# Kernel optimization log

Hardware: AMD Instinct MI355X
Metric: run time of the kernel (lower is better)

The kernel has to match this reference:

```python
import jax, jax.numpy as jnp
import numpy as np

B, D, H = 512, 32, 256
N_STEPS = 8
T0, T1 = 0.0, 1.0

# Dopri5 Butcher tableau (5th-order solution weights; k7 weight is 0 so 6 stages suffice)
_C = (0.0, 1.0 / 5, 3.0 / 10, 4.0 / 5, 8.0 / 9, 1.0)
_A = (
    (),
    (1.0 / 5,),
    (3.0 / 40, 9.0 / 40),
    (44.0 / 45, -56.0 / 15, 32.0 / 9),
    (19372.0 / 6561, -25360.0 / 2187, 64448.0 / 6561, -212.0 / 729),
    (9017.0 / 3168, -355.0 / 33, 46732.0 / 5247, 49.0 / 176, -5103.0 / 18656),
)
_B = (35.0 / 384, 0.0, 500.0 / 1113, 125.0 / 192, -2187.0 / 6784, 11.0 / 84)


def setup_inputs() -> dict:
    key = jax.random.key(0)
    ks = jax.random.split(key, 7)
    s1 = 1.0 / np.sqrt(D + 1)
    s2 = 1.0 / np.sqrt(H)
    return {
        "x": jax.random.normal(ks[0], (B, D), jnp.float32),
        "W1": (jax.random.normal(ks[1], (D + 1, H)) * s1).astype(jnp.float32),
        "b1": jnp.zeros((H,), jnp.float32),
        "W2": (jax.random.normal(ks[2], (H, H)) * s2).astype(jnp.float32),
        "b2": jnp.zeros((H,), jnp.float32),
        "W3": (jax.random.normal(ks[3], (H, D)) * s2).astype(jnp.float32),
        "b3": jnp.zeros((D,), jnp.float32),
    }


def _vf(t, x, W1, b1, W2, b2, W3, b3):
    # time-conditioned MLP vector field: input_shape == output_shape == (D,)
    h = jnp.concatenate([x, jnp.reshape(t, (1,)).astype(x.dtype)])
    h = jnp.tanh(h @ W1 + b1)
    h = jnp.tanh(h @ W2 + b2)
    return h @ W3 + b3


def _vf_and_trace(t, x, params):
    # exact Jacobian via D vmapped JVPs against identity, as in the original module
    apply_vf = lambda xx: _vf(t, xx, *params)
    eye = jnp.eye(D, dtype=x.dtype)
    dxdt_all, J = jax.vmap(lambda v: jax.jvp(apply_vf, (x,), (v,)))(eye)
    dxdt = dxdt_all[0]
    return dxdt, jnp.trace(J), jnp.sum(J * J)


def _deriv(t, carry, params):
    # forward (inverse=False) direction: t -> t1 - t, dxdt negated
    x, log_det, vf_norm, jac_frob = carry
    t_eff = T1 - t
    dxdt, tr, frob = jax.vmap(lambda xx: _vf_and_trace(t_eff, xx, params))(x)
    dxdt = -dxdt
    return (dxdt, -tr, jnp.sum(dxdt * dxdt, axis=-1), frob)


def _solve(x, params):
    dt = (T1 - T0) / N_STEPS
    zeros = jnp.zeros((x.shape[0],), x.dtype)
    y0 = (x, zeros, zeros, zeros)

    def step(carry, t):
        ks = []
        for i in range(6):
            if i == 0:
                yi = carry
            else:
                a = _A[i]
                yi = jax.tree_util.tree_map(
                    lambda y, *kk: y + dt * sum(c * k for c, k in zip(a, kk)),
                    carry, *ks)
            ks.append(_deriv(t + _C[i] * dt, yi, params))
        y_new = jax.tree_util.tree_map(
            lambda y, *kk: y + dt * sum(c * k for c, k in zip(_B, kk)),
            carry, *ks)
        return y_new, None

    ts = T0 + dt * jnp.arange(N_STEPS, dtype=x.dtype)
    (z, log_det, vf_norm, jac_frob), _ = jax.lax.scan(step, y0, ts)
    # pack (z, log_det, total_vf_norm, total_jac_frob_norm) into one array: (B, D+3)
    return jnp.concatenate(
        [z, log_det[:, None], vf_norm[:, None], jac_frob[:, None]], axis=-1)


def reference(x, W1, b1, W2, b2, W3, b3):
    return _solve(x, (W1, b1, W2, b2, W3, b3))
```

## Files before the change

kernel.cpp:

```cpp
#include <hip/hip_runtime.h>

#define NB 512
#define ND 32
#define NH 256
#define NSTEPS 8

typedef __attribute__((ext_vector_type(8))) short short8;
typedef __attribute__((ext_vector_type(4))) short short4v;
typedef __attribute__((ext_vector_type(4))) float f32x4;

__device__ __constant__ float Atab[6][5] = {
    {0.f, 0.f, 0.f, 0.f, 0.f},
    {0.2f, 0.f, 0.f, 0.f, 0.f},
    {3.f/40.f, 9.f/40.f, 0.f, 0.f, 0.f},
    {44.f/45.f, -56.f/15.f, 32.f/9.f, 0.f, 0.f},
    {19372.f/6561.f, -25360.f/2187.f, 64448.f/6561.f, -212.f/729.f, 0.f},
    {9017.f/3168.f, -355.f/33.f, 46732.f/5247.f, 49.f/176.f, -5103.f/18656.f}
};
__device__ __constant__ float Btab[6] = {
    35.f/384.f, 0.f, 500.f/1113.f, 125.f/192.f, -2187.f/6784.f, 11.f/84.f
};
__device__ __constant__ float Ctab[6] = {0.f, 0.2f, 0.3f, 0.8f, 8.f/9.f, 1.f};

static __device__ __forceinline__ short f2bf(float f){
    __bf16 h = (__bf16)f;
    return __builtin_bit_cast(short, h);
}
static __device__ __forceinline__ float bf_lo(unsigned p){
    return __builtin_bit_cast(float, p << 16);
}
static __device__ __forceinline__ float bf_hi(unsigned p){
    return __builtin_bit_cast(float, p & 0xffff0000u);
}
static __device__ __forceinline__ float fast_tanh(float x){
    float e = __expf(2.f * x);
    return 1.f - 2.f / (e + 1.f);
}

#define SWZ(base, row, byte) ((base) + ((row) << 9) + ((byte) ^ (((row) & 7) << 4)))

extern "C" __global__ void prep_kernel(const float* __restrict__ W3,
                                       short8* __restrict__ ws)
{
    const int tid = threadIdx.x;
    #pragma unroll
    for (int r = 0; r < 4; ++r) {
        const int idx = r*256 + tid;
        const int l  = idx & 63;
        const int kk = (idx >> 6) & 7;
        const int mt = idx >> 9;
        const int g = (l >> 4) & 3, c = l & 15;
        short8 v;
        #pragma unroll
        for (int e = 0; e < 8; ++e)
            v[e] = f2bf(W3[(kk*32 + g*8 + e)*ND + mt*16 + c]);
        ws[idx] = v;
    }
}

extern "C" __global__ void __launch_bounds__(256, 2)
node_kernel(const float* __restrict__ x_in,
            const float* __restrict__ W1, const float* __restrict__ b1,
            const float* __restrict__ W2, const float* __restrict__ b2,
            const float* __restrict__ W3, const float* __restrict__ b3,
            const short8* __restrict__ w3ws,
            float* __restrict__ out)
{
    __shared__ __align__(16) short LAA[33*256];
    __shared__ __align__(16) short LTs[33*256];
    __shared__ __align__(16) short8 W3L[16*64];
    __shared__ __align__(16) unsigned LW1[16*256];
    __shared__ __align__(16) float h2pre_s[NH];
    __shared__ __align__(16) float s2_s[NH];
    __shared__ __align__(16) float xs_s[4][ND];
    __shared__ __align__(16) float xc_s[4][ND];
    __shared__ __align__(16) float ksb[4][6][ND];
    __shared__ float red[4][3];

    const int bid = blockIdx.x;
    const int tid = threadIdx.x;
    const int w = tid >> 6;
    const int l = tid & 63;
    const int g = (tid >> 4) & 3;
    const int c = tid & 15;

    char* LAc = (char*)LAA;
    char* LTc = (char*)LTs;
    const int swc = (c & 7) << 4;

    short8 w2f[4][8];
    #pragma unroll
    for (int m = 0; m < 4; ++m) {
        const int j = w*64 + m*16 + c;
        #pragma unroll
        for (int kk = 0; kk < 8; ++kk) {
            const int k0 = kk*32 + g*8;
            short8 f;
            #pragma unroll
            for (int e = 0; e < 8; ++e) f[e] = f2bf(W2[(k0+e)*NH + j]);
            w2f[m][kk] = f;
        }
    }
    float w1t, b1u, b2u;
    {
        #pragma unroll
        for (int q = 0; q < 16; ++q) {
            unsigned lo = (unsigned)(unsigned short)f2bf(W1[(2*q)*NH + tid]);
            unsigned hi = (unsigned)(unsigned short)f2bf(W1[(2*q+1)*NH + tid]);
            LW1[q*256 + tid] = lo | (hi << 16);
        }
        w1t = W1[32*NH + tid];
        b1u = b1[tid];
        b2u = b2[tid];
    }
    const f32x4 b3a = *(const f32x4*)(b3 + g*4);
    const f32x4 b3b = *(const f32x4*)(b3 + 16 + g*4);
    #pragma unroll
    for (int r = 0; r < 4; ++r) W3L[r*256 + tid] = w3ws[r*256 + tid];
    const int mtJ = w >> 1, ntJ = w & 1;

    if (l < ND) {
        const float xv = x_in[bid*ND + l];
        xc_s[w][l] = xv;
        xs_s[w][l] = xv;
    }
    __syncthreads();

    const float dt = 0.125f;
    float fr_acc = 0.f, ld_acc = 0.f, vf_acc = 0.f;
    const short8 zfrag = {0,0,0,0,0,0,0,0};

    for (int n = 0; n < NSTEPS; ++n) {
        const float t0 = (float)n * dt;
        for (int sg = 0; sg < 6; ++sg) {
            const float t_eff = 1.0f - (t0 + Ctab[sg]*dt);

            {
                float pre = b1u + t_eff * w1t;
                #pragma unroll
                for (int q = 0; q < 8; ++q) {
                    f32x4 xq = *(const f32x4*)&xs_s[w][q*4];
                    unsigned p0 = LW1[(2*q)*256 + tid];
                    unsigned p1 = LW1[(2*q+1)*256 + tid];
                    pre += xq[0]*bf_lo(p0) + xq[1]*bf_hi(p0)
                         + xq[2]*bf_lo(p1) + xq[3]*bf_hi(p1);
                }
                const float h1 = fast_tanh(pre);
                const float s1 = 1.f - h1*h1;
                #pragma unroll
                for (int q = 0; q < 16; ++q) {
                    unsigned p = LW1[q*256 + tid];
                    *(short*)SWZ(LAc, 2*q,   2*tid) = f2bf(bf_lo(p)*s1);
                    *(short*)SWZ(LAc, 2*q+1, 2*tid) = f2bf(bf_hi(p)*s1);
                }
                ((short*)LAA)[32*256 + tid] = f2bf(h1);
            }
            __syncthreads();

            {
                f32x4 acc2[4];
                #pragma unroll
                for (int m = 0; m < 4; ++m) acc2[m] = (f32x4){0.f,0.f,0.f,0.f};
                #pragma unroll
                for (int kk = 0; kk < 8; ++kk) {
                    const int bo = kk*64 + g*16;
                    short8 fA2 = zfrag;
                    if (c == 0) fA2 = *(const short8*)(LAc + (32 << 9) + bo);
                    #pragma unroll
                    for (int m = 0; m < 4; ++m)
                        acc2[m] = __builtin_amdgcn_mfma_f32_16x16x32_bf16(w2f[m][kk], fA2, acc2[m], 0,0,0);
                }
                if (c == 0) {
                    #pragma unroll
                    for (int m = 0; m < 4; ++m)
                        *(f32x4*)&h2pre_s[w*64 + m*16 + g*4] = acc2[m];
                }
            }
            const float h2 = fast_tanh(h2pre_s[tid] + b2u);
            s2_s[tid] = 1.f - h2*h2;
            ((short*)LTs)[32*256 + tid] = f2bf(h2);

            #pragma unroll 1
            for (int nt = 0; nt < 2; ++nt) {
                f32x4 accT[4];
                #pragma unroll
                for (int m = 0; m < 4; ++m) accT[m] = (f32x4){0.f,0.f,0.f,0.f};
                #pragma unroll
                for (int kk = 0; kk < 8; ++kk) {
                    const int bo = kk*64 + g*16;
                    short8 fA = *(const short8*)(LAc + ((nt*16 + c) << 9) + (bo ^ swc));
                    #pragma unroll
                    for (int m = 0; m < 4; ++m)
                        accT[m] = __builtin_amdgcn_mfma_f32_16x16x32_bf16(w2f[m][kk], fA, accT[m], 0,0,0);
                }
                #pragma unroll
                for (int m = 0; m < 4; ++m) {
                    const int j0 = w*64 + m*16 + g*4;
                    f32x4 s2q = *(const f32x4*)&s2_s[j0];
                    f32x4 v = accT[m] * s2q;
                    short4v p;
                    p[0] = f2bf(v[0]); p[1] = f2bf(v[1]); p[2] = f2bf(v[2]); p[3] = f2bf(v[3]);
                    *(short4v*)SWZ(LTc, nt*16 + c, 2*j0) = p;
                }
            }
            __syncthreads();

            f32x4 jva = (f32x4){0,0,0,0}, jvb = (f32x4){0,0,0,0}, jj = (f32x4){0,0,0,0};
            #pragma unroll
            for (int kk = 0; kk < 8; ++kk) {
                const int bo = kk*64 + g*16;
                short8 w3f0 = W3L[kk*64 + l];
                short8 w3f1 = W3L[(8+kk)*64 + l];
                short8 h2f = zfrag;
                if (c == 0) h2f = *(const short8*)(LTc + (32 << 9) + bo);
                jva = __builtin_amdgcn_mfma_f32_16x16x32_bf16(w3f0, h2f, jva, 0,0,0);
                jvb = __builtin_amdgcn_mfma_f32_16x16x32_bf16(w3f1, h2f, jvb, 0,0,0);
                short8 bJ = *(const short8*)(LTc + ((ntJ*16 + c) << 9) + (bo ^ swc));
                jj = __builtin_amdgcn_mfma_f32_16x16x32_bf16((mtJ == 0) ? w3f0 : w3f1, bJ, jj, 0,0,0);
            }

            const float wB = dt * Btab[sg];
            if (c == 0) {
                f32x4 dxa, dxb;
                dxa[0] = -(jva[0]+b3a[0]); dxa[1] = -(jva[1]+b3a[1]);
                dxa[2] = -(jva[2]+b3a[2]); dxa[3] = -(jva[3]+b3a[3]);
                dxb[0] = -(jvb[0]+b3b[0]); dxb[1] = -(jvb[1]+b3b[1]);
                dxb[2] = -(jvb[2]+b3b[2]); dxb[3] = -(jvb[3]+b3b[3]);
                *(f32x4*)&ksb[w][sg][g*4]      = dxa;
                *(f32x4*)&ksb[w][sg][16 + g*4] = dxb;
                if (w == 3)
                    vf_acc += wB * (dxa[0]*dxa[0]+dxa[1]*dxa[1]+dxa[2]*dxa[2]+dxa[3]*dxa[3]
                                  + dxb[0]*dxb[0]+dxb[1]*dxb[1]+dxb[2]*dxb[2]+dxb[3]*dxb[3]);
            }
            if (l < ND) {
                if (sg < 5) {
                    float v = xc_s[w][l];
                    for (int q = 0; q <= sg; ++q) v += dt * Atab[sg+1][q] * ksb[w][q][l];
                    xs_s[w][l] = v;
                } else {
                    float v = xc_s[w][l];
                    #pragma unroll
                    for (int q = 0; q < 6; ++q) v += dt * Btab[q] * ksb[w][q][l];
                    xc_s[w][l] = v;
                    xs_s[w][l] = v;
                }
            }
            fr_acc += wB * (jj[0]*jj[0]+jj[1]*jj[1]+jj[2]*jj[2]+jj[3]*jj[3]);
            if (mtJ == ntJ) {
                const int dd = c - g*4;
                if (dd >= 0 && dd < 4) {
                    float da = (dd==0)?jj[0]:(dd==1)?jj[1]:(dd==2)?jj[2]:jj[3];
                    ld_acc -= wB * da;
                }
            }
        }
    }

    float fr = fr_acc, ld = ld_acc, vf = vf_acc;
    #pragma unroll
    for (int off = 32; off > 0; off >>= 1) {
        fr += __shfl_down(fr, off, 64);
        ld += __shfl_down(ld, off, 64);
        vf += __shfl_down(vf, off, 64);
    }
    if (l == 0) { red[w][0] = fr; red[w][1] = ld; red[w][2] = vf; }
    __syncthreads();
    if (tid == 0) {
        float a = 0.f, b = 0.f, cq = 0.f;
        #pragma unroll
        for (int q = 0; q < 4; ++q) { a += red[q][0]; b += red[q][1]; cq += red[q][2]; }
        out[bid*35 + 32] = b;
        out[bid*35 + 33] = cq;
        out[bid*35 + 34] = a;
    }
    if (w == 3 && l < ND) out[bid*35 + l] = xc_s[3][l];
}

extern "C" void kernel_launch(void* const* d_in, const int* in_sizes, int n_in,
                              void* d_out, int out_size, void* d_ws, size_t ws_size,
                              hipStream_t stream) {
    const float* x  = (const float*)d_in[0];
    const float* W1 = (const float*)d_in[1];
    const float* b1 = (const float*)d_in[2];
    const float* W2 = (const float*)d_in[3];
    const float* b2 = (const float*)d_in[4];
    const float* W3 = (const float*)d_in[5];
    const float* b3 = (const float*)d_in[6];
    float* outp = (float*)d_out;
    hipLaunchKernelGGL(prep_kernel, dim3(1), dim3(256), 0, stream,
                       W3, (short8*)d_ws);
    hipLaunchKernelGGL(node_kernel, dim3(NB), dim3(256), 0, stream,
                       x, W1, b1, W2, b2, W3, b3, (const short8*)d_ws, outp);
}
```

Measured before the change: 219.0 us.

## Process two samples per block with software-pipelined interleaved RK stages

Each block now handles two batch samples instead of one and interleaves their RK stage phases (alpha, beta1, beta2), so one sample's elementwise work overlaps the other's MFMA work between barriers. Shared buffers are doubled per sample, W3 fragments move from LDS into registers, and the grid is halved with launch bounds set to one block per SM. This aims to cut barrier stalls and serial dependency latency per stage. In exchange it raises register and LDS pressure and halves the grid to 256 blocks, which may leave CUs underused.

```diff
diff --git a/kernel.cpp b/kernel.cpp
--- a/kernel.cpp
+++ b/kernel.cpp
@@ -58,7 +58,7 @@
     }
 }
 
-extern "C" __global__ void __launch_bounds__(256, 2)
+extern "C" __global__ void __launch_bounds__(256, 1)
 node_kernel(const float* __restrict__ x_in,
             const float* __restrict__ W1, const float* __restrict__ b1,
             const float* __restrict__ W2, const float* __restrict__ b2,
@@ -66,16 +66,15 @@
             const short8* __restrict__ w3ws,
             float* __restrict__ out)
 {
-    __shared__ __align__(16) short LAA[33*256];
-    __shared__ __align__(16) short LTs[33*256];
-    __shared__ __align__(16) short8 W3L[16*64];
+    __shared__ __align__(16) short LAA[2][33*256];
+    __shared__ __align__(16) short LTs[2][33*256];
     __shared__ __align__(16) unsigned LW1[16*256];
-    __shared__ __align__(16) float h2pre_s[NH];
-    __shared__ __align__(16) float s2_s[NH];
-    __shared__ __align__(16) float xs_s[4][ND];
-    __shared__ __align__(16) float xc_s[4][ND];
-    __shared__ __align__(16) float ksb[4][6][ND];
-    __shared__ float red[4][3];
+    __shared__ __align__(16) float h2p[2][NH];
+    __shared__ __align__(16) float s2s[2][NH];
+    __shared__ __align__(16) float xss[4][2][ND];
+    __shared__ __align__(16) float xcs[4][2][ND];
+    __shared__ __align__(16) float ksb[4][2][6][ND];
+    __shared__ float red[4][6];
 
     const int bid = blockIdx.x;
     const int tid = threadIdx.x;
@@ -84,8 +83,6 @@
     const int g = (tid >> 4) & 3;
     const int c = tid & 15;
 
-    char* LAc = (char*)LAA;
-    char* LTc = (char*)LTs;
     const int swc = (c & 7) << 4;
 
     short8 w2f[4][8];
@@ -115,165 +112,202 @@
     }
     const f32x4 b3a = *(const f32x4*)(b3 + g*4);
     const f32x4 b3b = *(const f32x4*)(b3 + 16 + g*4);
+    short8 w3f0[8], w3f1[8];
     #pragma unroll
-    for (int r = 0; r < 4; ++r) W3L[r*256 + tid] = w3ws[r*256 + tid];
+    for (int kk = 0; kk < 8; ++kk) {
+        w3f0[kk] = w3ws[kk*64 + l];
+        w3f1[kk] = w3ws[(8+kk)*64 + l];
+    }
     const int mtJ = w >> 1, ntJ = w & 1;
 
     if (l < ND) {
-        const float xv = x_in[bid*ND + l];
-        xc_s[w][l] = xv;
-        xs_s[w][l] = xv;
+        const float x0 = x_in[(2*bid+0)*ND + l];
+        const float x1 = x_in[(2*bid+1)*ND + l];
+        xcs[w][0][l] = x0; xss[w][0][l] = x0;
+        xcs[w][1][l] = x1; xss[w][1][l] = x1;
     }
     __syncthreads();
 
     const float dt = 0.125f;
-    float fr_acc = 0.f, ld_acc = 0.f, vf_acc = 0.f;
+    float fr_a[2] = {0.f, 0.f}, ld_a[2] = {0.f, 0.f}, vf_a[2] = {0.f, 0.f};
     const short8 zfrag = {0,0,0,0,0,0,0,0};
 
-    for (int n = 0; n < NSTEPS; ++n) {
-        const float t0 = (float)n * dt;
-        for (int sg = 0; sg < 6; ++sg) {
-            const float t_eff = 1.0f - (t0 + Ctab[sg]*dt);
-
-            {
-                float pre = b1u + t_eff * w1t;
-                #pragma unroll
-                for (int q = 0; q < 8; ++q) {
-                    f32x4 xq = *(const f32x4*)&xs_s[w][q*4];
-                    unsigned p0 = LW1[(2*q)*256 + tid];
-                    unsigned p1 = LW1[(2*q+1)*256 + tid];
-                    pre += xq[0]*bf_lo(p0) + xq[1]*bf_hi(p0)
-                         + xq[2]*bf_lo(p1) + xq[3]*bf_hi(p1);
-                }
-                const float h1 = fast_tanh(pre);
-                const float s1 = 1.f - h1*h1;
-                #pragma unroll
-                for (int q = 0; q < 16; ++q) {
-                    unsigned p = LW1[q*256 + tid];
-                    *(short*)SWZ(LAc, 2*q,   2*tid) = f2bf(bf_lo(p)*s1);
-                    *(short*)SWZ(LAc, 2*q+1, 2*tid) = f2bf(bf_hi(p)*s1);
-                }
-                ((short*)LAA)[32*256 + tid] = f2bf(h1);
-            }
-            __syncthreads();
-
-            {
-                f32x4 acc2[4];
-                #pragma unroll
-                for (int m = 0; m < 4; ++m) acc2[m] = (f32x4){0.f,0.f,0.f,0.f};
-                #pragma unroll
-                for (int kk = 0; kk < 8; ++kk) {
-                    const int bo = kk*64 + g*16;
-                    short8 fA2 = zfrag;
-                    if (c == 0) fA2 = *(const short8*)(LAc + (32 << 9) + bo);
-                    #pragma unroll
-                    for (int m = 0; m < 4; ++m)
-                        acc2[m] = __builtin_amdgcn_mfma_f32_16x16x32_bf16(w2f[m][kk], fA2, acc2[m], 0,0,0);
-                }
-                if (c == 0) {
-                    #pragma unroll
-                    for (int m = 0; m < 4; ++m)
-                        *(f32x4*)&h2pre_s[w*64 + m*16 + g*4] = acc2[m];
-                }
-            }
-            const float h2 = fast_tanh(h2pre_s[tid] + b2u);
-            s2_s[tid] = 1.f - h2*h2;
-            ((short*)LTs)[32*256 + tid] = f2bf(h2);
-
-            #pragma unroll 1
-            for (int nt = 0; nt < 2; ++nt) {
-                f32x4 accT[4];
-                #pragma unroll
-                for (int m = 0; m < 4; ++m) accT[m] = (f32x4){0.f,0.f,0.f,0.f};
-                #pragma unroll
-                for (int kk = 0; kk < 8; ++kk) {
-                    const int bo = kk*64 + g*16;
-                    short8 fA = *(const short8*)(LAc + ((nt*16 + c) << 9) + (bo ^ swc));
-                    #pragma unroll
-                    for (int m = 0; m < 4; ++m)
-                        accT[m] = __builtin_amdgcn_mfma_f32_16x16x32_bf16(w2f[m][kk], fA, accT[m], 0,0,0);
-                }
-                #pragma unroll
-                for (int m = 0; m < 4; ++m) {
-                    const int j0 = w*64 + m*16 + g*4;
-                    f32x4 s2q = *(const f32x4*)&s2_s[j0];
-                    f32x4 v = accT[m] * s2q;
-                    short4v p;
-                    p[0] = f2bf(v[0]); p[1] = f2bf(v[1]); p[2] = f2bf(v[2]); p[3] = f2bf(v[3]);
-                    *(short4v*)SWZ(LTc, nt*16 + c, 2*j0) = p;
-                }
-            }
-            __syncthreads();
-
-            f32x4 jva = (f32x4){0,0,0,0}, jvb = (f32x4){0,0,0,0}, jj = (f32x4){0,0,0,0};
+    auto alpha = [&](int e, float t_eff) {
+        char* LAc = (char*)LAA[e];
+        float pre = b1u + t_eff * w1t;
+        #pragma unroll
+        for (int q = 0; q < 8; ++q) {
+            f32x4 xq = *(const f32x4*)&xss[w][e][q*4];
+            unsigned p0 = LW1[(2*q)*256 + tid];
+            unsigned p1 = LW1[(2*q+1)*256 + tid];
+            pre += xq[0]*bf_lo(p0) + xq[1]*bf_hi(p0)
+                 + xq[2]*bf_lo(p1) + xq[3]*bf_hi(p1);
+        }
+        const float h1 = fast_tanh(pre);
+        const float s1 = 1.f - h1*h1;
+        #pragma unroll
+        for (int q = 0; q < 16; ++q) {
+            unsigned p = LW1[q*256 + tid];
+            *(short*)SWZ(LAc, 2*q,   2*tid) = f2bf(bf_lo(p)*s1);
+            *(short*)SWZ(LAc, 2*q+1, 2*tid) = f2bf(bf_hi(p)*s1);
+        }
+        ((short*)LAA[e])[32*256 + tid] = f2bf(h1);
+    };
+
+    auto beta1 = [&](int e) {
+        char* LAc = (char*)LAA[e];
+        char* LTc = (char*)LTs[e];
+        {
+            f32x4 acc2[4];
+            #pragma unroll
+            for (int m = 0; m < 4; ++m) acc2[m] = (f32x4){0.f,0.f,0.f,0.f};
             #pragma unroll
             for (int kk = 0; kk < 8; ++kk) {
                 const int bo = kk*64 + g*16;
-                short8 w3f0 = W3L[kk*64 + l];
-                short8 w3f1 = W3L[(8+kk)*64 + l];
-                short8 h2f = zfrag;
-                if (c == 0) h2f = *(const short8*)(LTc + (32 << 9) + bo);
-                jva = __builtin_amdgcn_mfma_f32_16x16x32_bf16(w3f0, h2f, jva, 0,0,0);
-                jvb = __builtin_amdgcn_mfma_f32_16x16x32_bf16(w3f1, h2f, jvb, 0,0,0);
-                short8 bJ = *(const short8*)(LTc + ((ntJ*16 + c) << 9) + (bo ^ swc));
-                jj = __builtin_amdgcn_mfma_f32_16x16x32_bf16((mtJ == 0) ? w3f0 : w3f1, bJ, jj, 0,0,0);
-            }
-
-            const float wB = dt * Btab[sg];
+                short8 fA2 = zfrag;
+                if (c == 0) fA2 = *(const short8*)(LAc + (32 << 9) + bo);
+                #pragma unroll
+                for (int m = 0; m < 4; ++m)
+                    acc2[m] = __builtin_amdgcn_mfma_f32_16x16x32_bf16(w2f[m][kk], fA2, acc2[m], 0,0,0);
+            }
             if (c == 0) {
-                f32x4 dxa, dxb;
-                dxa[0] = -(jva[0]+b3a[0]); dxa[1] = -(jva[1]+b3a[1]);
-                dxa[2] = -(jva[2]+b3a[2]); dxa[3] = -(jva[3]+b3a[3]);
-                dxb[0] = -(jvb[0]+b3b[0]); dxb[1] = -(jvb[1]+b3b[1]);
-                dxb[2] = -(jvb[2]+b3b[2]); dxb[3] = -(jvb[3]+b3b[3]);
-                *(f32x4*)&ksb[w][sg][g*4]      = dxa;
-                *(f32x4*)&ksb[w][sg][16 + g*4] = dxb;
-                if (w == 3)
-                    vf_acc += wB * (dxa[0]*dxa[0]+dxa[1]*dxa[1]+dxa[2]*dxa[2]+dxa[3]*dxa[3]
-                                  + dxb[0]*dxb[0]+dxb[1]*dxb[1]+dxb[2]*dxb[2]+dxb[3]*dxb[3]);
-            }
-            if (l < ND) {
-                if (sg < 5) {
-                    float v = xc_s[w][l];
-                    for (int q = 0; q <= sg; ++q) v += dt * Atab[sg+1][q] * ksb[w][q][l];
-                    xs_s[w][l] = v;
-                } else {
-                    float v = xc_s[w][l];
-                    #pragma unroll
-                    for (int q = 0; q < 6; ++q) v += dt * Btab[q] * ksb[w][q][l];
-                    xc_s[w][l] = v;
-                    xs_s[w][l] = v;
-                }
-            }
-            fr_acc += wB * (jj[0]*jj[0]+jj[1]*jj[1]+jj[2]*jj[2]+jj[3]*jj[3]);
-            if (mtJ == ntJ) {
-                const int dd = c - g*4;
-                if (dd >= 0 && dd < 4) {
-                    float da = (dd==0)?jj[0]:(dd==1)?jj[1]:(dd==2)?jj[2]:jj[3];
-                    ld_acc -= wB * da;
-                }
-            }
-        }
-    }
-
-    float fr = fr_acc, ld = ld_acc, vf = vf_acc;
+                #pragma unroll
+                for (int m = 0; m < 4; ++m)
+                    *(f32x4*)&h2p[e][w*64 + m*16 + g*4] = acc2[m];
+            }
+        }
+        const float h2 = fast_tanh(h2p[e][tid] + b2u);
+        s2s[e][tid] = 1.f - h2*h2;
+        ((short*)LTs[e])[32*256 + tid] = f2bf(h2);
+        #pragma unroll 1
+        for (int nt = 0; nt < 2; ++nt) {
+            f32x4 accT[4];
+            #pragma unroll
+            for (int m = 0; m < 4; ++m) accT[m] = (f32x4){0.f,0.f,0.f,0.f};
+            #pragma unroll
+            for (int kk = 0; kk < 8; ++kk) {
+                const int bo = kk*64 + g*16;
+                short8 fA = *(const short8*)(LAc + ((nt*16 + c) << 9) + (bo ^ swc));
+                #pragma unroll
+                for (int m = 0; m < 4; ++m)
+                    accT[m] = __builtin_amdgcn_mfma_f32_16x16x32_bf16(w2f[m][kk], fA, accT[m], 0,0,0);
+            }
+            #pragma unroll
+            for (int m = 0; m < 4; ++m) {
+                const int j0 = w*64 + m*16 + g*4;
+                f32x4 s2q = *(const f32x4*)&s2s[e][j0];
+                f32x4 v = accT[m] * s2q;
+                short4v p;
+                p[0] = f2bf(v[0]); p[1] = f2bf(v[1]); p[2] = f2bf(v[2]); p[3] = f2bf(v[3]);
+                *(short4v*)SWZ(LTc, nt*16 + c, 2*j0) = p;
+            }
+        }
+    };
+
+    auto beta2 = [&](int e, int sg, float wB) {
+        char* LTc = (char*)LTs[e];
+        f32x4 jva = (f32x4){0,0,0,0}, jvb = (f32x4){0,0,0,0}, jj = (f32x4){0,0,0,0};
+        #pragma unroll
+        for (int kk = 0; kk < 8; ++kk) {
+            const int bo = kk*64 + g*16;
+            short8 h2f = zfrag;
+            if (c == 0) h2f = *(const short8*)(LTc + (32 << 9) + bo);
+            jva = __builtin_amdgcn_mfma_f32_16x16x32_bf16(w3f0[kk], h2f, jva, 0,0,0);
+            jvb = __builtin_amdgcn_mfma_f32_16x16x32_bf16(w3f1[kk], h2f, jvb, 0,0,0);
+            short8 bJ = *(const short8*)(LTc + ((ntJ*16 + c) << 9) + (bo ^ swc));
+            jj = __builtin_amdgcn_mfma_f32_16x16x32_bf16((mtJ == 0) ? w3f0[kk] : w3f1[kk], bJ, jj, 0,0,0);
+        }
+        if (c == 0) {
+            f32x4 dxa, dxb;
+            dxa[0] = -(jva[0]+b3a[0]); dxa[1] = -(jva[1]+b3a[1]);
+            dxa[2] = -(jva[2]+b3a[2]); dxa[3] = -(jva[3]+b3a[3]);
+            dxb[0] = -(jvb[0]+b3b[0]); dxb[1] = -(jvb[1]+b3b[1]);
+            dxb[2] = -(jvb[2]+b3b[2]); dxb[3] = -(jvb[3]+b3b[3]);
+            *(f32x4*)&ksb[w][e][sg][g*4]      = dxa;
+            *(f32x4*)&ksb[w][e][sg][16 + g*4] = dxb;
+            if (w == 3)
+                vf_a[e] += wB * (dxa[0]*dxa[0]+dxa[1]*dxa[1]+dxa[2]*dxa[2]+dxa[3]*dxa[3]
+                               + dxb[0]*dxb[0]+dxb[1]*dxb[1]+dxb[2]*dxb[2]+dxb[3]*dxb[3]);
+        }
+        if (l < ND) {
+            if (sg < 5) {
+                float v = xcs[w][e][l];
+                for (int q = 0; q <= sg; ++q) v += dt * Atab[sg+1][q] * ksb[w][e][q][l];
+                xss[w][e][l] = v;
+            } else {
+                float v = xcs[w][e][l];
+                #pragma unroll
+                for (int q = 0; q < 6; ++q) v += dt * Btab[q] * ksb[w][e][q][l];
+                xcs[w][e][l] = v;
+                xss[w][e][l] = v;
+            }
+        }
+        fr_a[e] += wB * (jj[0]*jj[0]+jj[1]*jj[1]+jj[2]*jj[2]+jj[3]*jj[3]);
+        if (mtJ == ntJ) {
+            const int dd = c - g*4;
+            if (dd >= 0 && dd < 4) {
+                float da = (dd==0)?jj[0]:(dd==1)?jj[1]:(dd==2)?jj[2]:jj[3];
+                ld_a[e] -= wB * da;
+            }
+        }
+    };
+
+    auto teff_of = [&](int s) {
+        const int n = s / 6, sg = s % 6;
+        return 1.0f - ((float)n * dt + Ctab[sg] * dt);
+    };
+
+    alpha(0, teff_of(0));
+    __syncthreads();
+    #pragma unroll 1
+    for (int s = 0; s < NSTEPS*6; ++s) {
+        const int sg = s % 6;
+        const float wB = dt * Btab[sg];
+        if (s > 0) beta2(1, (s-1) % 6, dt * Btab[(s-1) % 6]);
+        alpha(1, teff_of(s));
+        beta1(0);
+        __syncthreads();
+        beta2(0, sg, wB);
+        if (s < NSTEPS*6 - 1) alpha(0, teff_of(s+1));
+        beta1(1);
+        __syncthreads();
+    }
+    beta2(1, 5, dt * Btab[5]);
+
+    float r0 = fr_a[0], r1 = ld_a[0], r2 = vf_a[0];
+    float r3 = fr_a[1], r4 = ld_a[1], r5 = vf_a[1];
     #pragma unroll
     for (int off = 32; off > 0; off >>= 1) {
-        fr += __shfl_down(fr, off, 64);
-        ld += __shfl_down(ld, off, 64);
-        vf += __shfl_down(vf, off, 64);
-    }
-    if (l == 0) { red[w][0] = fr; red[w][1] = ld; red[w][2] = vf; }
+        r0 += __shfl_down(r0, off, 64);
+        r1 += __shfl_down(r1, off, 64);
+        r2 += __shfl_down(r2, off, 64);
+        r3 += __shfl_down(r3, off, 64);
+        r4 += __shfl_down(r4, off, 64);
+        r5 += __shfl_down(r5, off, 64);
+    }
+    if (l == 0) {
+        red[w][0]=r0; red[w][1]=r1; red[w][2]=r2;
+        red[w][3]=r3; red[w][4]=r4; red[w][5]=r5;
+    }
     __syncthreads();
     if (tid == 0) {
-        float a = 0.f, b = 0.f, cq = 0.f;
-        #pragma unroll
-        for (int q = 0; q < 4; ++q) { a += red[q][0]; b += red[q][1]; cq += red[q][2]; }
-        out[bid*35 + 32] = b;
-        out[bid*35 + 33] = cq;
-        out[bid*35 + 34] = a;
-    }
-    if (w == 3 && l < ND) out[bid*35 + l] = xc_s[3][l];
+        float a0=0,b0=0,c0=0,a1=0,b1v=0,c1=0;
+        #pragma unroll
+        for (int q = 0; q < 4; ++q) {
+            a0+=red[q][0]; b0+=red[q][1]; c0+=red[q][2];
+            a1+=red[q][3]; b1v+=red[q][4]; c1+=red[q][5];
+        }
+        out[(2*bid+0)*35 + 32] = b0;
+        out[(2*bid+0)*35 + 33] = c0;
+        out[(2*bid+0)*35 + 34] = a0;
+        out[(2*bid+1)*35 + 32] = b1v;
+        out[(2*bid+1)*35 + 33] = c1;
+        out[(2*bid+1)*35 + 34] = a1;
+    }
+    if (w == 3 && l < ND) {
+        out[(2*bid+0)*35 + l] = xcs[3][0][l];
+        out[(2*bid+1)*35 + l] = xcs[3][1][l];
+    }
 }
 
 extern "C" void kernel_launch(void* const* d_in, const int* in_sizes, int n_in,
@@ -289,6 +323,6 @@
     float* outp = (float*)d_out;
     hipLaunchKernelGGL(prep_kernel, dim3(1), dim3(256), 0, stream,
                        W3, (short8*)d_ws);
-    hipLaunchKernelGGL(node_kernel, dim3(NB), dim3(256), 0, stream,
+    hipLaunchKernelGGL(node_kernel, dim3(NB/2), dim3(256), 0, stream,
                        x, W1, b1, W2, b2, W3, b3, (const short8*)d_ws, outp);
 }
```

After: 347.0 us. 1.58x slower.
